# Performance work log

Measured on AMD Instinct MI355X. Metric: run time of the kernel, lower is better.

## Reference

```python
import jax, jax.numpy as jnp
import numpy as np

WINDOW_SIZE = 3
SIGMA = 1.5
C1 = 0.01 ** 2
C2 = 0.03 ** 2


def gaussian_window(channel, window_size=WINDOW_SIZE, sigma=SIGMA):
    x = jnp.arange(window_size, dtype=jnp.float32) - window_size // 2
    g1 = jnp.exp(-(x ** 2) / (2.0 * sigma ** 2))
    g1 = g1 / g1.sum()
    g2 = jnp.outer(g1, g1)  # [k, k]
    # depthwise kernel OIHW: [C, 1, k, k]
    return jnp.broadcast_to(g2, (channel, 1, window_size, window_size))


def depthwise_conv(x, window, channel, window_size=WINDOW_SIZE):
    pad = window_size // 2
    return jax.lax.conv_general_dilated(
        x, window,
        window_strides=(1, 1),
        padding=((pad, pad), (pad, pad)),
        dimension_numbers=('NCHW', 'OIHW', 'NCHW'),
        feature_group_count=channel,
    )


def setup_inputs() -> dict:
    key = jax.random.key(0)
    k1, k2 = jax.random.split(key)
    img1 = jax.random.uniform(k1, (32, 3, 512, 512), dtype=jnp.float32)
    img2 = jax.random.uniform(k2, (32, 3, 512, 512), dtype=jnp.float32)
    return {"img1": img1, "img2": img2}


def reference(img1, img2):
    channel = img1.shape[1]
    window = gaussian_window(channel)

    mu1 = depthwise_conv(img1, window, channel)
    mu2 = depthwise_conv(img2, window, channel)
    mu1_sq = mu1 * mu1
    mu2_sq = mu2 * mu2
    mu1_mu2 = mu1 * mu2

    sigma1_sq = depthwise_conv(img1 * img1, window, channel) - mu1_sq
    sigma2_sq = depthwise_conv(img2 * img2, window, channel) - mu2_sq
    sigma12 = depthwise_conv(img1 * img2, window, channel) - mu1_mu2

    ssim_map = ((2.0 * mu1_mu2 + C1) * (2.0 * sigma12 + C2)) / (
        (mu1_sq + mu2_sq + C1) * (sigma1_sq + sigma2_sq + C2))

    # size_sum defaults to True inside ssim() -> scalar sum
    return 1.0 - ssim_map.sum()
```

## Files before the change

### kernel.cpp

```cpp
#include <hip/hip_runtime.h>

#define IMG_H 512
#define IMG_W 512
#define RH 32

__global__ void ssim_init_kernel(double* __restrict__ accum) {
    if (threadIdx.x == 0 && blockIdx.x == 0) *accum = 0.0;
}

__global__ __launch_bounds__(256) void ssim_main_kernel(
    const float* __restrict__ img1, const float* __restrict__ img2,
    double* __restrict__ accum)
{
    constexpr float W_E = 0.30780133f;
    constexpr float W_C = 0.38439734f;
    constexpr float C1 = 1e-4f;
    constexpr float C2 = 9e-4f;

    const int t = threadIdx.x;
    const int y0 = blockIdx.x * RH;
    const size_t base = (size_t)blockIdx.y * (IMG_H * IMG_W);
    const float* __restrict__ A = img1 + base;
    const float* __restrict__ B = img2 + base;

    __shared__ __align__(16) float lsA[2][520];
    __shared__ __align__(16) float lsB[2][520];
    if (t < 2) {
        lsA[0][t * 513] = 0.0f; lsA[1][t * 513] = 0.0f;
        lsB[0][t * 513] = 0.0f; lsB[1][t * 513] = 0.0f;
    }

    const int x = 2 * t;

    float h1[2][3], h2[2][3], h11[2][3], h22[2][3], h12[2][3];
#pragma unroll
    for (int c = 0; c < 2; ++c)
#pragma unroll
        for (int r = 0; r < 3; ++r) {
            h1[c][r] = 0.f; h2[c][r] = 0.f;
            h11[c][r] = 0.f; h22[c][r] = 0.f; h12[c][r] = 0.f;
        }

    float2 pa = make_float2(0.f, 0.f), pb = make_float2(0.f, 0.f);
    {
        const int yi = y0 - 1;
        if (yi >= 0) {
            pa = *(const float2*)(A + (size_t)yi * IMG_W + x);
            pb = *(const float2*)(B + (size_t)yi * IMG_W + x);
        }
    }

    float tsum = 0.0f;

    for (int i = 0; i < RH + 2; ++i) {
        const int buf = i & 1;
        lsA[buf][1 + x] = pa.x; lsA[buf][2 + x] = pa.y;
        lsB[buf][1 + x] = pb.x; lsB[buf][2 + x] = pb.y;

        const int yn = y0 + i;
        float2 na = make_float2(0.f, 0.f), nb = make_float2(0.f, 0.f);
        if (i + 1 < RH + 2 && yn < IMG_H) {
            na = *(const float2*)(A + (size_t)yn * IMG_W + x);
            nb = *(const float2*)(B + (size_t)yn * IMG_W + x);
        }

        __syncthreads();

        const float2 a01 = *(const float2*)&lsA[buf][x];
        const float2 a23 = *(const float2*)&lsA[buf][x + 2];
        const float2 b01 = *(const float2*)&lsB[buf][x];
        const float2 b23 = *(const float2*)&lsB[buf][x + 2];
        const float av[4] = {a01.x, a01.y, a23.x, a23.y};
        const float bv[4] = {b01.x, b01.y, b23.x, b23.y};

#pragma unroll
        for (int c = 0; c < 2; ++c) {
            h1[c][0] = h1[c][1];  h1[c][1] = h1[c][2];
            h2[c][0] = h2[c][1];  h2[c][1] = h2[c][2];
            h11[c][0] = h11[c][1]; h11[c][1] = h11[c][2];
            h22[c][0] = h22[c][1]; h22[c][1] = h22[c][2];
            h12[c][0] = h12[c][1]; h12[c][1] = h12[c][2];
            const float am = av[c], a0 = av[c + 1], ap = av[c + 2];
            const float bm = bv[c], b0 = bv[c + 1], bp = bv[c + 2];
            h1[c][2]  = W_E * (am + ap) + W_C * a0;
            h2[c][2]  = W_E * (bm + bp) + W_C * b0;
            h11[c][2] = W_E * (am * am + ap * ap) + W_C * (a0 * a0);
            h22[c][2] = W_E * (bm * bm + bp * bp) + W_C * (b0 * b0);
            h12[c][2] = W_E * (am * bm + ap * bp) + W_C * (a0 * b0);
        }

        if (i >= 2) {
#pragma unroll
            for (int c = 0; c < 2; ++c) {
                const float mu1 = W_E * (h1[c][0] + h1[c][2]) + W_C * h1[c][1];
                const float mu2 = W_E * (h2[c][0] + h2[c][2]) + W_C * h2[c][1];
                const float e11 = W_E * (h11[c][0] + h11[c][2]) + W_C * h11[c][1];
                const float e22 = W_E * (h22[c][0] + h22[c][2]) + W_C * h22[c][1];
                const float e12 = W_E * (h12[c][0] + h12[c][2]) + W_C * h12[c][1];
                const float mu1s = mu1 * mu1, mu2s = mu2 * mu2, m12 = mu1 * mu2;
                const float s11 = e11 - mu1s, s22 = e22 - mu2s, s12 = e12 - m12;
                const float num = (2.0f * m12 + C1) * (2.0f * s12 + C2);
                const float den = (mu1s + mu2s + C1) * (s11 + s22 + C2);
                tsum += num / den;
            }
        }

        pa = na; pb = nb;
    }

#pragma unroll
    for (int off = 32; off >= 1; off >>= 1)
        tsum += __shfl_xor(tsum, off, 64);

    __shared__ float wpart[4];
    if ((t & 63) == 0) wpart[t >> 6] = tsum;
    __syncthreads();
    if (t == 0) {
        const double bs = (double)wpart[0] + (double)wpart[1] +
                          (double)wpart[2] + (double)wpart[3];
        atomicAdd(accum, bs);
    }
}

__global__ void ssim_fin_kernel(const double* __restrict__ accum,
                                float* __restrict__ out) {
    if (threadIdx.x == 0 && blockIdx.x == 0) out[0] = 1.0f - (float)(*accum);
}

extern "C" void kernel_launch(void* const* d_in, const int* in_sizes, int n_in,
                              void* d_out, int out_size, void* d_ws, size_t ws_size,
                              hipStream_t stream) {
    const float* img1 = (const float*)d_in[0];
    const float* img2 = (const float*)d_in[1];
    float* out = (float*)d_out;
    double* accum = (double*)d_ws;

    const int planes = in_sizes[0] / (IMG_H * IMG_W);

    ssim_init_kernel<<<1, 1, 0, stream>>>(accum);
    dim3 grid(IMG_H / RH, planes);
    ssim_main_kernel<<<grid, 256, 0, stream>>>(img1, img2, accum);
    ssim_fin_kernel<<<1, 1, 0, stream>>>(accum, out);
}
```

Baseline: 228.5 us.

## Give each wavefront one row-strip, with neighbours exchanged via shuffles instead of LDS

Each wavefront now owns a 16-row strip of one plane and covers the full 512-pixel width, 8 columns per lane. It keeps a rotating 4-row register window loaded with float4 reads. Horizontal halo values come from lane shuffles rather than shared memory plus __syncthreads, and the division becomes a hardware reciprocal. The single global atomic is spread over 64 padded slots, which a wavefront-shuffle finish kernel sums. This trades higher register pressure and more halo-row re-reads (strips are 16 rows instead of 32) for no block barriers, and the approximate reciprocal slightly changes numerics.

```diff
diff --git a/kernel.cpp b/kernel.cpp
--- a/kernel.cpp
+++ b/kernel.cpp
@@ -2,129 +2,137 @@
 
 #define IMG_H 512
 #define IMG_W 512
-#define RH 32
+#define RH 16
+#define STRIPS (IMG_H / RH)
+#define PLANE_N (IMG_H * IMG_W)
+#define NSLOT 64
+#define SLOT_STRIDE 8
+
+constexpr float W_E = 0.30780133f;
+constexpr float W_C = 0.38439734f;
+constexpr float C1v = 1e-4f;
+constexpr float C2v = 9e-4f;
+
+struct RowRegs { float a[8]; float b[8]; };
+
+__device__ __forceinline__ void load_row(const float* __restrict__ A,
+                                         const float* __restrict__ B,
+                                         int row, int col0, RowRegs& s) {
+    if ((unsigned)row < IMG_H) {
+        const float* pa = A + (size_t)row * IMG_W + col0;
+        const float* pb = B + (size_t)row * IMG_W + col0;
+        const float4 a0 = ((const float4*)pa)[0];
+        const float4 a1 = ((const float4*)pa)[1];
+        const float4 b0 = ((const float4*)pb)[0];
+        const float4 b1 = ((const float4*)pb)[1];
+        s.a[0] = a0.x; s.a[1] = a0.y; s.a[2] = a0.z; s.a[3] = a0.w;
+        s.a[4] = a1.x; s.a[5] = a1.y; s.a[6] = a1.z; s.a[7] = a1.w;
+        s.b[0] = b0.x; s.b[1] = b0.y; s.b[2] = b0.z; s.b[3] = b0.w;
+        s.b[4] = b1.x; s.b[5] = b1.y; s.b[6] = b1.z; s.b[7] = b1.w;
+    } else {
+#pragma unroll
+        for (int c = 0; c < 8; ++c) { s.a[c] = 0.f; s.b[c] = 0.f; }
+    }
+}
+
+__device__ __forceinline__ float wsum3(float m, float c, float p) {
+    return fmaf(W_E, m + p, W_C * c);
+}
+
+__device__ __forceinline__ float ssim_out_row(const RowRegs& r0, const RowRegs& r1,
+                                              const RowRegs& r2,
+                                              bool lane0, bool lane63) {
+    float v1[8], v2[8], q11[8], q22[8], q12[8];
+#pragma unroll
+    for (int c = 0; c < 8; ++c) {
+        const float a0 = r0.a[c], a1 = r1.a[c], a2 = r2.a[c];
+        const float b0 = r0.b[c], b1 = r1.b[c], b2 = r2.b[c];
+        v1[c]  = wsum3(a0, a1, a2);
+        v2[c]  = wsum3(b0, b1, b2);
+        q11[c] = fmaf(W_E, fmaf(a0, a0, a2 * a2), W_C * (a1 * a1));
+        q22[c] = fmaf(W_E, fmaf(b0, b0, b2 * b2), W_C * (b1 * b1));
+        q12[c] = fmaf(W_E, fmaf(a0, b0, a2 * b2), W_C * (a1 * b1));
+    }
+    float L1  = __shfl_up(v1[7], 1);    if (lane0)  L1  = 0.f;
+    float L2  = __shfl_up(v2[7], 1);    if (lane0)  L2  = 0.f;
+    float L11 = __shfl_up(q11[7], 1);   if (lane0)  L11 = 0.f;
+    float L22 = __shfl_up(q22[7], 1);   if (lane0)  L22 = 0.f;
+    float L12 = __shfl_up(q12[7], 1);   if (lane0)  L12 = 0.f;
+    float R1  = __shfl_down(v1[0], 1);  if (lane63) R1  = 0.f;
+    float R2  = __shfl_down(v2[0], 1);  if (lane63) R2  = 0.f;
+    float R11 = __shfl_down(q11[0], 1); if (lane63) R11 = 0.f;
+    float R22 = __shfl_down(q22[0], 1); if (lane63) R22 = 0.f;
+    float R12 = __shfl_down(q12[0], 1); if (lane63) R12 = 0.f;
+
+    float sum = 0.f;
+#pragma unroll
+    for (int c = 0; c < 8; ++c) {
+        const float m1  = wsum3(c ? v1[c-1]  : L1,  v1[c],  c < 7 ? v1[c+1]  : R1);
+        const float m2  = wsum3(c ? v2[c-1]  : L2,  v2[c],  c < 7 ? v2[c+1]  : R2);
+        const float e11 = wsum3(c ? q11[c-1] : L11, q11[c], c < 7 ? q11[c+1] : R11);
+        const float e22 = wsum3(c ? q22[c-1] : L22, q22[c], c < 7 ? q22[c+1] : R22);
+        const float e12 = wsum3(c ? q12[c-1] : L12, q12[c], c < 7 ? q12[c+1] : R12);
+        const float mu1s = m1 * m1, mu2s = m2 * m2, m12 = m1 * m2;
+        const float s11 = e11 - mu1s, s22 = e22 - mu2s, s12 = e12 - m12;
+        const float num = fmaf(2.f, m12, C1v) * fmaf(2.f, s12, C2v);
+        const float den = (mu1s + mu2s + C1v) * (s11 + s22 + C2v);
+        sum = fmaf(num, __builtin_amdgcn_rcpf(den), sum);
+    }
+    return sum;
+}
 
 __global__ void ssim_init_kernel(double* __restrict__ accum) {
-    if (threadIdx.x == 0 && blockIdx.x == 0) *accum = 0.0;
+    const int i = blockIdx.x * blockDim.x + threadIdx.x;
+    if (i < NSLOT * SLOT_STRIDE) accum[i] = 0.0;
 }
 
-__global__ __launch_bounds__(256) void ssim_main_kernel(
+__global__ __launch_bounds__(256, 3) void ssim_main_kernel(
     const float* __restrict__ img1, const float* __restrict__ img2,
     double* __restrict__ accum)
 {
-    constexpr float W_E = 0.30780133f;
-    constexpr float W_C = 0.38439734f;
-    constexpr float C1 = 1e-4f;
-    constexpr float C2 = 9e-4f;
+    const int t = threadIdx.x;
+    const int lane = t & 63;
+    const int task = blockIdx.x * 4 + (t >> 6);
+    const int plane = task >> 5;
+    const int y0 = (task & 31) * RH;
+    const int col0 = lane << 3;
+    const bool lane0 = (lane == 0), lane63 = (lane == 63);
+    const float* __restrict__ A = img1 + (size_t)plane * PLANE_N;
+    const float* __restrict__ B = img2 + (size_t)plane * PLANE_N;
 
-    const int t = threadIdx.x;
-    const int y0 = blockIdx.x * RH;
-    const size_t base = (size_t)blockIdx.y * (IMG_H * IMG_W);
-    const float* __restrict__ A = img1 + base;
-    const float* __restrict__ B = img2 + base;
+    RowRegs s0, s1, s2, s3;
+    load_row(A, B, y0 - 1, col0, s0);
+    load_row(A, B, y0,     col0, s1);
+    load_row(A, B, y0 + 1, col0, s2);
+    load_row(A, B, y0 + 2, col0, s3);
 
-    __shared__ __align__(16) float lsA[2][520];
-    __shared__ __align__(16) float lsB[2][520];
-    if (t < 2) {
-        lsA[0][t * 513] = 0.0f; lsA[1][t * 513] = 0.0f;
-        lsB[0][t * 513] = 0.0f; lsB[1][t * 513] = 0.0f;
-    }
-
-    const int x = 2 * t;
-
-    float h1[2][3], h2[2][3], h11[2][3], h22[2][3], h12[2][3];
-#pragma unroll
-    for (int c = 0; c < 2; ++c)
-#pragma unroll
-        for (int r = 0; r < 3; ++r) {
-            h1[c][r] = 0.f; h2[c][r] = 0.f;
-            h11[c][r] = 0.f; h22[c][r] = 0.f; h12[c][r] = 0.f;
-        }
-
-    float2 pa = make_float2(0.f, 0.f), pb = make_float2(0.f, 0.f);
-    {
-        const int yi = y0 - 1;
-        if (yi >= 0) {
-            pa = *(const float2*)(A + (size_t)yi * IMG_W + x);
-            pb = *(const float2*)(B + (size_t)yi * IMG_W + x);
-        }
-    }
-
-    float tsum = 0.0f;
-
-    for (int i = 0; i < RH + 2; ++i) {
-        const int buf = i & 1;
-        lsA[buf][1 + x] = pa.x; lsA[buf][2 + x] = pa.y;
-        lsB[buf][1 + x] = pb.x; lsB[buf][2 + x] = pb.y;
-
-        const int yn = y0 + i;
-        float2 na = make_float2(0.f, 0.f), nb = make_float2(0.f, 0.f);
-        if (i + 1 < RH + 2 && yn < IMG_H) {
-            na = *(const float2*)(A + (size_t)yn * IMG_W + x);
-            nb = *(const float2*)(B + (size_t)yn * IMG_W + x);
-        }
-
-        __syncthreads();
-
-        const float2 a01 = *(const float2*)&lsA[buf][x];
-        const float2 a23 = *(const float2*)&lsA[buf][x + 2];
-        const float2 b01 = *(const float2*)&lsB[buf][x];
-        const float2 b23 = *(const float2*)&lsB[buf][x + 2];
-        const float av[4] = {a01.x, a01.y, a23.x, a23.y};
-        const float bv[4] = {b01.x, b01.y, b23.x, b23.y};
-
-#pragma unroll
-        for (int c = 0; c < 2; ++c) {
-            h1[c][0] = h1[c][1];  h1[c][1] = h1[c][2];
-            h2[c][0] = h2[c][1];  h2[c][1] = h2[c][2];
-            h11[c][0] = h11[c][1]; h11[c][1] = h11[c][2];
-            h22[c][0] = h22[c][1]; h22[c][1] = h22[c][2];
-            h12[c][0] = h12[c][1]; h12[c][1] = h12[c][2];
-            const float am = av[c], a0 = av[c + 1], ap = av[c + 2];
-            const float bm = bv[c], b0 = bv[c + 1], bp = bv[c + 2];
-            h1[c][2]  = W_E * (am + ap) + W_C * a0;
-            h2[c][2]  = W_E * (bm + bp) + W_C * b0;
-            h11[c][2] = W_E * (am * am + ap * ap) + W_C * (a0 * a0);
-            h22[c][2] = W_E * (bm * bm + bp * bp) + W_C * (b0 * b0);
-            h12[c][2] = W_E * (am * bm + ap * bp) + W_C * (a0 * b0);
-        }
-
-        if (i >= 2) {
-#pragma unroll
-            for (int c = 0; c < 2; ++c) {
-                const float mu1 = W_E * (h1[c][0] + h1[c][2]) + W_C * h1[c][1];
-                const float mu2 = W_E * (h2[c][0] + h2[c][2]) + W_C * h2[c][1];
-                const float e11 = W_E * (h11[c][0] + h11[c][2]) + W_C * h11[c][1];
-                const float e22 = W_E * (h22[c][0] + h22[c][2]) + W_C * h22[c][1];
-                const float e12 = W_E * (h12[c][0] + h12[c][2]) + W_C * h12[c][1];
-                const float mu1s = mu1 * mu1, mu2s = mu2 * mu2, m12 = mu1 * mu2;
-                const float s11 = e11 - mu1s, s22 = e22 - mu2s, s12 = e12 - m12;
-                const float num = (2.0f * m12 + C1) * (2.0f * s12 + C2);
-                const float den = (mu1s + mu2s + C1) * (s11 + s22 + C2);
-                tsum += num / den;
-            }
-        }
-
-        pa = na; pb = nb;
+    float tsum = 0.f;
+#pragma unroll 1
+    for (int m = 0; m < RH; m += 4) {
+        const int yo = y0 + m;
+        tsum += ssim_out_row(s0, s1, s2, lane0, lane63);
+        load_row(A, B, yo + 3, col0, s0);
+        tsum += ssim_out_row(s1, s2, s3, lane0, lane63);
+        load_row(A, B, yo + 4, col0, s1);
+        tsum += ssim_out_row(s2, s3, s0, lane0, lane63);
+        load_row(A, B, yo + 5, col0, s2);
+        tsum += ssim_out_row(s3, s0, s1, lane0, lane63);
+        load_row(A, B, yo + 6, col0, s3);
     }
 
 #pragma unroll
-    for (int off = 32; off >= 1; off >>= 1)
-        tsum += __shfl_xor(tsum, off, 64);
-
-    __shared__ float wpart[4];
-    if ((t & 63) == 0) wpart[t >> 6] = tsum;
-    __syncthreads();
-    if (t == 0) {
-        const double bs = (double)wpart[0] + (double)wpart[1] +
-                          (double)wpart[2] + (double)wpart[3];
-        atomicAdd(accum, bs);
-    }
+    for (int off = 32; off; off >>= 1) tsum += __shfl_xor(tsum, off, 64);
+    if (lane == 0)
+        atomicAdd(&accum[(task & (NSLOT - 1)) * SLOT_STRIDE], (double)tsum);
 }
 
 __global__ void ssim_fin_kernel(const double* __restrict__ accum,
                                 float* __restrict__ out) {
-    if (threadIdx.x == 0 && blockIdx.x == 0) out[0] = 1.0f - (float)(*accum);
+    const int lane = threadIdx.x;
+    double v = accum[lane * SLOT_STRIDE];
+#pragma unroll
+    for (int off = 32; off; off >>= 1) v += __shfl_xor(v, off, 64);
+    if (lane == 0) out[0] = 1.0f - (float)v;
 }
 
 extern "C" void kernel_launch(void* const* d_in, const int* in_sizes, int n_in,
@@ -135,10 +143,11 @@
     float* out = (float*)d_out;
     double* accum = (double*)d_ws;
 
-    const int planes = in_sizes[0] / (IMG_H * IMG_W);
+    const int planes = in_sizes[0] / PLANE_N;
+    const int tasks = planes * STRIPS;
+    const int blocks = tasks / 4;
 
-    ssim_init_kernel<<<1, 1, 0, stream>>>(accum);
-    dim3 grid(IMG_H / RH, planes);
-    ssim_main_kernel<<<grid, 256, 0, stream>>>(img1, img2, accum);
-    ssim_fin_kernel<<<1, 1, 0, stream>>>(accum, out);
+    ssim_init_kernel<<<2, 256, 0, stream>>>(accum);
+    ssim_main_kernel<<<blocks, 256, 0, stream>>>(img1, img2, accum);
+    ssim_fin_kernel<<<1, 64, 0, stream>>>(accum, out);
 }
```

Result: slower. 317.3 us (+38.9%).
